# Optimization experiments

Hardware: AMD Instinct MI355X
Metric: run time of the kernel (lower is better)

The kernel has to match this reference:

```python
import jax, jax.numpy as jnp
import numpy as np

THRESHOLD = 1.0  # max tolerable Sampson error (px^2), as in the docstring example scale


def _normalize(pts, w):
    # pts: (B, M, 3) homogeneous points, w: (B, M) 0/1 weights.
    # Hartley normalization: centroid -> origin, mean distance -> sqrt(2).
    ws = w.sum(-1, keepdims=True)                                   # (B, 1)
    mean = (pts[..., :2] * w[..., None]).sum(-2) / ws               # (B, 2)
    d = jnp.linalg.norm(pts[..., :2] - mean[..., None, :], axis=-1)  # (B, M)
    md = (d * w).sum(-1) / ws[..., 0]                               # (B,)
    s = jnp.sqrt(2.0) / (md + 1e-8)
    z, o = jnp.zeros_like(s), jnp.ones_like(s)
    T = jnp.stack([
        jnp.stack([s, z, -s * mean[..., 0]], -1),
        jnp.stack([z, s, -s * mean[..., 1]], -1),
        jnp.stack([z, z, o], -1)], -2)                              # (B, 3, 3)
    return pts @ jnp.swapaxes(T, -1, -2), T


def eight_point(p1, p2, w):
    # Weighted normalized 8-point algorithm. p1, p2: (B, M, 3); w: (B, M).
    # Zero-weight rows contribute nothing to A^T A, so this equals fitting on the
    # selected subset (as the original does by fancy-indexing inlier rows).
    p1n, T1 = _normalize(p1, w)
    p2n, T2 = _normalize(p2, w)
    A = (p2n[..., :, None] * p1n[..., None, :]).reshape(p1.shape[:-2] + (-1, 9))
    A = A * w[..., None]                                            # (B, M, 9)
    AtA = jnp.einsum('...mi,...mj->...ij', A, A)                    # (B, 9, 9)
    _, V = jnp.linalg.eigh(AtA)                                     # ascending eigvals
    F = V[..., :, 0].reshape(p1.shape[:-2] + (3, 3))                # null vector
    U, S, Vt = jnp.linalg.svd(F, full_matrices=False)               # enforce rank 2
    F = (U * S.at[..., -1].set(0.0)[..., None, :]) @ Vt
    F = jnp.swapaxes(T2, -1, -2) @ F @ T1                           # denormalize
    return F / F[..., 2:3, 2:3]


def sampson_error(p1, p2, F):
    # p1, p2: (N, 3); F: (B, 3, 3) -> err: (B, N)
    Fx1 = jnp.einsum('bij,nj->bni', F, p1)
    Ftx2 = jnp.einsum('bij,ni->bnj', F, p2)
    num = jnp.einsum('ni,bni->bn', p2, Fx1) ** 2
    den = Fx1[..., 0] ** 2 + Fx1[..., 1] ** 2 + Ftx2[..., 0] ** 2 + Ftx2[..., 1] ** 2
    return num / den


def setup_inputs() -> dict:
    N, ITERS, K = 16384, 4096, 8
    rng = np.random.default_rng(0)
    X = rng.uniform(-2.0, 2.0, (N, 3)); X[:, 2] += 6.0               # 3D points, depth ~[4, 8]
    Kmat = np.array([[500.0, 0.0, 256.0], [0.0, 500.0, 256.0], [0.0, 0.0, 1.0]])
    th = 0.1
    R = np.array([[np.cos(th), 0.0, np.sin(th)], [0.0, 1.0, 0.0], [-np.sin(th), 0.0, np.cos(th)]])
    t = np.array([0.5, 0.1, 0.0])
    x1 = X @ Kmat.T; x1 /= x1[:, 2:]
    X2 = X @ R.T + t
    x2 = X2 @ Kmat.T; x2 /= x2[:, 2:]
    x1[:, :2] += rng.normal(0.0, 0.3, (N, 2))
    x2[:, :2] += rng.normal(0.0, 0.3, (N, 2))
    out = rng.random(N) < 0.3
    x2[out, :2] = rng.uniform(0.0, 512.0, (int(out.sum()), 2))
    samples = jax.random.randint(jax.random.key(0), (ITERS, K), 0, N, dtype=jnp.int32)
    return {"pts1": jnp.asarray(x1, jnp.float32), "pts2": jnp.asarray(x2, jnp.float32),
            "samples": samples, "iterations": ITERS, "num_of_select": K}


def reference(pts1, pts2, samples, iterations, num_of_select):
    samples = samples[:iterations, :num_of_select]                   # (B, 8), static slice
    # uniqueness check per hypothesis row (original drops non-unique rows; we mask them)
    srt = jnp.sort(samples, axis=-1)
    uniq = jnp.all(srt[:, 1:] != srt[:, :-1], axis=-1)               # (B,)
    p1s, p2s = pts1[samples], pts2[samples]                          # (B, 8, 3)
    w1 = jnp.ones(samples.shape, pts1.dtype)
    F = eight_point(p1s, p2s, w1)                                    # (B, 3, 3)
    err = sampson_error(pts1, pts2, F)                               # (B, N)
    inl = err <= THRESHOLD
    ml = inl.sum(-1).astype(pts1.dtype)                              # mask_lens
    ml_max = jnp.max(jnp.where(uniq, ml, 0.0))
    mask_len_ratio = ml / ml_max
    # sqrt of inlier errors; safe-guard masked entries so sqrt grad stays finite
    sqrt_sum = (jnp.sqrt(jnp.where(inl, err, 1.0)) * inl).sum(-1)
    means = (sqrt_sum + 1e-8) / (ml + 1e-8)
    means_max = jnp.max(jnp.where(uniq, means, -jnp.inf))
    score = 0.5 * mask_len_ratio + 0.5 * (1.0 - means / means_max)
    best = jnp.argmax(jnp.where(uniq, score, -jnp.inf))
    wbest = inl[best].astype(pts1.dtype)                             # (N,)
    Mbest = eight_point(pts1[None], pts2[None], wbest[None])[0]      # refit on inliers
    return Mbest, inl[best]
```

## Files before the change

### kernel.cpp

```cpp
#include <hip/hip_runtime.h>
#include <math.h>
#include <type_traits>
#include <utility>

#if defined(__has_builtin)
#if __has_builtin(__builtin_amdgcn_rcpf)
#define FAST_RCPF(x) __builtin_amdgcn_rcpf(x)
#endif
#if __has_builtin(__builtin_amdgcn_sqrtf)
#define FAST_SQRTF(x) __builtin_amdgcn_sqrtf(x)
#endif
#endif
#ifndef FAST_RCPF
#define FAST_RCPF(x) (1.0f / (x))
#endif
#ifndef FAST_SQRTF
#define FAST_SQRTF(x) sqrtf(x)
#endif

__host__ __device__ constexpr int PIX(int i, int j) { return i * (i + 1) / 2 + j; }

template <int N, int I = 0, typename F>
__device__ __forceinline__ void static_for(F&& f) {
  if constexpr (I < N) {
    f(std::integral_constant<int, I>{});
    static_for<N, I + 1>(static_cast<F&&>(f));
  }
}

template <int I, int J, int K>
__device__ __forceinline__ double csub9(const double* M, double s) {
  if constexpr (K >= J) return s;
  else return csub9<I, J, K + 1>(M, s - M[PIX(I, K)] * M[PIX(J, K)]);
}
template <int I, int J>
__device__ __forceinline__ void cholJ(double* M) {
  if constexpr (J <= I) {
    double s = csub9<I, J, 0>(M, M[PIX(I, J)]);
    if constexpr (J == I)
      M[PIX(I, I)] = sqrt(fmax(s, 1e-300));
    else
      M[PIX(I, J)] = s / M[PIX(J, J)];
    cholJ<I, J + 1>(M);
  }
}
template <int I>
__device__ __forceinline__ void cholI(double* M) {
  if constexpr (I < 9) {
    cholJ<I, 0>(M);
    cholI<I + 1>(M);
  }
}

template <int I, int K>
__device__ __forceinline__ double fsub9(const double* L, const double* x, double s) {
  if constexpr (K >= I) return s;
  else return fsub9<I, K + 1>(L, x, s - L[PIX(I, K)] * x[K]);
}
template <int I>
__device__ __forceinline__ void fwd9(const double* L, double* x) {
  if constexpr (I < 9) {
    x[I] = fsub9<I, 0>(L, x, x[I]) / L[PIX(I, I)];
    fwd9<I + 1>(L, x);
  }
}
template <int I, int K>
__device__ __forceinline__ double bsub9(const double* L, const double* x, double s) {
  if constexpr (K >= 9) return s;
  else return bsub9<I, K + 1>(L, x, s - L[PIX(K, I)] * x[K]);
}
template <int I>
__device__ __forceinline__ void bwd9(const double* L, double* x) {
  if constexpr (I >= 0) {
    x[I] = bsub9<I, I + 1>(L, x, x[I]) / L[PIX(I, I)];
    bwd9<I - 1>(L, x);
  }
}

template <int I, int J>
__device__ __forceinline__ void ataIJ(double* M, const double (&a)[9], double w) {
  if constexpr (J <= I) {
    M[PIX(I, J)] += w * a[I] * a[J];
    ataIJ<I, J + 1>(M, a, w);
  }
}
template <int I>
__device__ __forceinline__ void ataI(double* M, const double (&a)[9], double w) {
  if constexpr (I < 9) {
    ataIJ<I, 0>(M, a, w);
    ataI<I + 1>(M, a, w);
  }
}

#define JROT(P, Q)                                                              \
  {                                                                             \
    double apq = a##P##Q;                                                       \
    if (fabs(apq) >= 1e-300) {                                                  \
      double tau = (a##Q##Q - a##P##P) / (2.0 * apq);                           \
      double t = ((tau >= 0.0) ? 1.0 : -1.0) / (fabs(tau) + sqrt(1.0 + tau * tau)); \
      double c = 1.0 / sqrt(1.0 + t * t);                                       \
      double s = t * c;                                                         \
      double t0p = a0##P, t0q = a0##Q;                                          \
      a0##P = c * t0p - s * t0q; a0##Q = s * t0p + c * t0q;                     \
      double t1p = a1##P, t1q = a1##Q;                                          \
      a1##P = c * t1p - s * t1q; a1##Q = s * t1p + c * t1q;                     \
      double t2p = a2##P, t2q = a2##Q;                                          \
      a2##P = c * t2p - s * t2q; a2##Q = s * t2p + c * t2q;                     \
      double rp0 = a##P##0, rq0 = a##Q##0;                                      \
      a##P##0 = c * rp0 - s * rq0; a##Q##0 = s * rp0 + c * rq0;                 \
      double rp1 = a##P##1, rq1 = a##Q##1;                                      \
      a##P##1 = c * rp1 - s * rq1; a##Q##1 = s * rp1 + c * rq1;                 \
      double rp2 = a##P##2, rq2 = a##Q##2;                                      \
      a##P##2 = c * rp2 - s * rq2; a##Q##2 = s * rp2 + c * rq2;                 \
      double u0p = V0##P, u0q = V0##Q;                                          \
      V0##P = c * u0p - s * u0q; V0##Q = s * u0p + c * u0q;                     \
      double u1p = V1##P, u1q = V1##Q;                                          \
      V1##P = c * u1p - s * u1q; V1##Q = s * u1p + c * u1q;                     \
      double u2p = V2##P, u2q = V2##Q;                                          \
      V2##P = c * u2p - s * u2q; V2##Q = s * u2p + c * u2q;                     \
    }                                                                           \
  }

__device__ __forceinline__ void solveF(double* M, double s1, double m1x, double m1y,
                                       double s2, double m2x, double m2y,
                                       float* out) {
  double tr = M[0] + M[2] + M[5] + M[9] + M[14] + M[20] + M[27] + M[35] + M[44];
  double shift = 1e-12 * tr;
  M[0] += shift; M[2] += shift; M[5] += shift; M[9] += shift; M[14] += shift;
  M[20] += shift; M[27] += shift; M[35] += shift; M[44] += shift;
  cholI<0>(M);
  double x[9];
  static_for<9>([&](auto i) { x[i] = 1.0; });
  static_for<3>([&](auto) {
    fwd9<0>(M, x);
    bwd9<8>(M, x);
    double n = 0.0;
    static_for<9>([&](auto i) { n += x[i] * x[i]; });
    n = 1.0 / sqrt(n);
    static_for<9>([&](auto i) { x[i] *= n; });
  });
  const double g00 = x[0] * x[0] + x[3] * x[3] + x[6] * x[6];
  const double g01 = x[0] * x[1] + x[3] * x[4] + x[6] * x[7];
  const double g02 = x[0] * x[2] + x[3] * x[5] + x[6] * x[8];
  const double g11 = x[1] * x[1] + x[4] * x[4] + x[7] * x[7];
  const double g12 = x[1] * x[2] + x[4] * x[5] + x[7] * x[8];
  const double g22 = x[2] * x[2] + x[5] * x[5] + x[8] * x[8];
  double a00 = g00, a01 = g01, a02 = g02;
  double a10 = g01, a11 = g11, a12 = g12;
  double a20 = g02, a21 = g12, a22 = g22;
  double V00 = 1, V01 = 0, V02 = 0;
  double V10 = 0, V11 = 1, V12 = 0;
  double V20 = 0, V21 = 0, V22 = 1;
  for (int sweep = 0; sweep < 6; ++sweep) {
    JROT(0, 1);
    JROT(0, 2);
    JROT(1, 2);
  }
  double mv = a00, v0 = V00, v1 = V10, v2 = V20;
  if (a11 < mv) { mv = a11; v0 = V01; v1 = V11; v2 = V21; }
  if (a22 < mv) { mv = a22; v0 = V02; v1 = V12; v2 = V22; }
  const double fv0 = x[0] * v0 + x[1] * v1 + x[2] * v2;
  const double fv1 = x[3] * v0 + x[4] * v1 + x[5] * v2;
  const double fv2 = x[6] * v0 + x[7] * v1 + x[8] * v2;
  const double F200 = x[0] - fv0 * v0, F201 = x[1] - fv0 * v1, F202 = x[2] - fv0 * v2;
  const double F210 = x[3] - fv1 * v0, F211 = x[4] - fv1 * v1, F212 = x[5] - fv1 * v2;
  const double F220 = x[6] - fv2 * v0, F221 = x[7] - fv2 * v1, F222 = x[8] - fv2 * v2;
  const double R00 = s2 * F200, R01 = s2 * F201, R02 = s2 * F202;
  const double R10 = s2 * F210, R11 = s2 * F211, R12 = s2 * F212;
  const double R20 = -s2 * m2x * F200 - s2 * m2y * F210 + F220;
  const double R21 = -s2 * m2x * F201 - s2 * m2y * F211 + F221;
  const double R22 = -s2 * m2x * F202 - s2 * m2y * F212 + F222;
  const double Ff00 = s1 * R00, Ff01 = s1 * R01;
  const double Ff02 = -s1 * m1x * R00 - s1 * m1y * R01 + R02;
  const double Ff10 = s1 * R10, Ff11 = s1 * R11;
  const double Ff12 = -s1 * m1x * R10 - s1 * m1y * R11 + R12;
  const double Ff20 = s1 * R20, Ff21 = s1 * R21;
  const double Ff22 = -s1 * m1x * R20 - s1 * m1y * R21 + R22;
  const double inv = 1.0 / Ff22;
  out[0] = (float)(Ff00 * inv); out[1] = (float)(Ff01 * inv); out[2] = (float)(Ff02 * inv);
  out[3] = (float)(Ff10 * inv); out[4] = (float)(Ff11 * inv); out[5] = (float)(Ff12 * inv);
  out[6] = (float)(Ff20 * inv); out[7] = (float)(Ff21 * inv); out[8] = (float)(Ff22 * inv);
}

struct F9 {
  float f0, f1, f2, f3, f4, f5, f6, f7, f8;
};

__device__ __forceinline__ F9 loadF(const float* __restrict__ p) {
  F9 F;
  F.f0 = p[0]; F.f1 = p[1]; F.f2 = p[2];
  F.f3 = p[3]; F.f4 = p[4]; F.f5 = p[5];
  F.f6 = p[6]; F.f7 = p[7]; F.f8 = p[8];
  return F;
}

__device__ __forceinline__ void samp_numden(const F9& F, float px, float py,
                                            float qx, float qy, float& num,
                                            float& den) {
  float a0 = fmaf(F.f0, px, fmaf(F.f1, py, F.f2));
  float a1 = fmaf(F.f3, px, fmaf(F.f4, py, F.f5));
  float a2 = fmaf(F.f6, px, fmaf(F.f7, py, F.f8));
  float b0 = fmaf(F.f0, qx, fmaf(F.f3, qy, F.f6));
  float b1 = fmaf(F.f1, qx, fmaf(F.f4, qy, F.f7));
  float d = fmaf(qx, a0, fmaf(qy, a1, a2));
  num = d * d;
  den = fmaf(a0, a0, fmaf(a1, a1, fmaf(b0, b0, b1 * b1)));
}

__device__ __forceinline__ void samp_acc(const F9& F, float px, float py,
                                         float qx, float qy, float& cnt,
                                         float& ss) {
  float num, den;
  samp_numden(F, px, py, qx, qy, num, den);
  if (num <= den) {
    cnt += 1.0f;
    ss += FAST_SQRTF(num * FAST_RCPF(den));
  }
}

__global__ __launch_bounds__(256, 1) void prep_and_fit(
    const float* __restrict__ pts1, const float* __restrict__ pts2,
    const int* __restrict__ samples, float4* __restrict__ P1,
    float4* __restrict__ P2, float* __restrict__ models,
    int* __restrict__ uflag, int N, int iters, int TB) {
  if ((int)blockIdx.x < TB) {
    const int i = blockIdx.x * 256 + threadIdx.x;
    if (i < N) {
      P1[i] = make_float4(pts1[3 * i], pts1[3 * i + 1], pts1[3 * i + 2], 0.f);
      P2[i] = make_float4(pts2[3 * i], pts2[3 * i + 1], pts2[3 * i + 2], 0.f);
    }
    return;
  }
  if (threadIdx.x >= 64) return;
  const int it = (blockIdx.x - TB) * 64 + threadIdx.x;
  if (it >= iters) return;

  int idx[8];
  static_for<8>([&](auto k) { idx[k] = samples[it * 8 + k]; });
  int u = 1;
  static_for<8>([&](auto A) {
    static_for<8>([&](auto B) {
      if constexpr (decltype(B)::value > decltype(A)::value) {
        if (idx[A] == idx[B]) u = 0;
      }
    });
  });
  uflag[it] = u;

  float X1[8], Y1[8], Z1[8], X2[8], Y2[8], Z2[8];
  static_for<8>([&](auto k) {
    const int j = idx[k];
    X1[k] = pts1[3 * j]; Y1[k] = pts1[3 * j + 1]; Z1[k] = pts1[3 * j + 2];
    X2[k] = pts2[3 * j]; Y2[k] = pts2[3 * j + 1]; Z2[k] = pts2[3 * j + 2];
  });
  double sx1 = 0, sy1 = 0, sx2 = 0, sy2 = 0;
  static_for<8>([&](auto k) {
    sx1 += (double)X1[k]; sy1 += (double)Y1[k];
    sx2 += (double)X2[k]; sy2 += (double)Y2[k];
  });
  const double m1x = sx1 / 8.0, m1y = sy1 / 8.0;
  const double m2x = sx2 / 8.0, m2y = sy2 / 8.0;
  double sd1 = 0, sd2 = 0;
  static_for<8>([&](auto k) {
    double dx1 = (double)X1[k] - m1x, dy1 = (double)Y1[k] - m1y;
    double dx2 = (double)X2[k] - m2x, dy2 = (double)Y2[k] - m2y;
    sd1 += sqrt(dx1 * dx1 + dy1 * dy1);
    sd2 += sqrt(dx2 * dx2 + dy2 * dy2);
  });
  const double s1 = sqrt(2.0) / (sd1 / 8.0 + 1e-8);
  const double s2 = sqrt(2.0) / (sd2 / 8.0 + 1e-8);

  double M[45];
  static_for<45>([&](auto r) { M[r] = 0.0; });
  static_for<8>([&](auto k) {
    const double z1 = (double)Z1[k], z2 = (double)Z2[k];
    const double p1x = s1 * ((double)X1[k] - m1x * z1);
    const double p1y = s1 * ((double)Y1[k] - m1y * z1);
    const double p2x = s2 * ((double)X2[k] - m2x * z2);
    const double p2y = s2 * ((double)Y2[k] - m2y * z2);
    const double a[9] = {p2x * p1x, p2x * p1y, p2x * z1,
                         p2y * p1x, p2y * p1y, p2y * z1,
                         z2 * p1x,  z2 * p1y,  z2 * z1};
    ataI<0>(M, a, 1.0);
  });
  solveF(M, s1, m1x, m1y, s2, m2x, m2y, models + (size_t)it * 9);
}

__global__ __launch_bounds__(256, 4) void sampson_stats4(
    const float4* __restrict__ P1, const float4* __restrict__ P2,
    const float* __restrict__ models, float* __restrict__ ml,
    float* __restrict__ ssum, int N, int iters) {
  const int m0 = blockIdx.x * 4;
  const int c0 = min(m0 + 0, iters - 1), c1 = min(m0 + 1, iters - 1);
  const int c2 = min(m0 + 2, iters - 1), c3 = min(m0 + 3, iters - 1);
  const F9 Fa = loadF(models + (size_t)c0 * 9);
  const F9 Fb = loadF(models + (size_t)c1 * 9);
  const F9 Fc = loadF(models + (size_t)c2 * 9);
  const F9 Fd = loadF(models + (size_t)c3 * 9);
  float ca = 0, cb = 0, cc = 0, cd = 0;
  float sa = 0, sb = 0, sc_ = 0, sd = 0;
  const int NP = N & ~511;
  for (int i = threadIdx.x; i < NP; i += 512) {
    const float4 pA = P1[i];
    const float4 qA = P2[i];
    const float4 pB = P1[i + 256];
    const float4 qB = P2[i + 256];
    samp_acc(Fa, pA.x, pA.y, qA.x, qA.y, ca, sa);
    samp_acc(Fb, pA.x, pA.y, qA.x, qA.y, cb, sb);
    samp_acc(Fc, pA.x, pA.y, qA.x, qA.y, cc, sc_);
    samp_acc(Fd, pA.x, pA.y, qA.x, qA.y, cd, sd);
    samp_acc(Fa, pB.x, pB.y, qB.x, qB.y, ca, sa);
    samp_acc(Fb, pB.x, pB.y, qB.x, qB.y, cb, sb);
    samp_acc(Fc, pB.x, pB.y, qB.x, qB.y, cc, sc_);
    samp_acc(Fd, pB.x, pB.y, qB.x, qB.y, cd, sd);
  }
  for (int i = NP + threadIdx.x; i < N; i += 256) {
    const float4 p = P1[i];
    const float4 q = P2[i];
    samp_acc(Fa, p.x, p.y, q.x, q.y, ca, sa);
    samp_acc(Fb, p.x, p.y, q.x, q.y, cb, sb);
    samp_acc(Fc, p.x, p.y, q.x, q.y, cc, sc_);
    samp_acc(Fd, p.x, p.y, q.x, q.y, cd, sd);
  }
  __shared__ float shc[4][4], shs[4][4];
  const int lane = threadIdx.x & 63, wv = threadIdx.x >> 6;
  float c4[4] = {ca, cb, cc, cd};
  float s4[4] = {sa, sb, sc_, sd};
  static_for<4>([&](auto m) {
    float c = c4[m], s = s4[m];
#pragma unroll
    for (int o = 32; o > 0; o >>= 1) {
      c += __shfl_down(c, o);
      s += __shfl_down(s, o);
    }
    if (lane == 0) { shc[wv][m] = c; shs[wv][m] = s; }
  });
  __syncthreads();
  if (threadIdx.x < 4 && m0 + threadIdx.x < iters) {
    const int m = threadIdx.x;
    ml[m0 + m] = shc[0][m] + shc[1][m] + shc[2][m] + shc[3][m];
    ssum[m0 + m] = shs[0][m] + shs[1][m] + shs[2][m] + shs[3][m];
  }
}

__global__ __launch_bounds__(256) void select_best(
    const float* __restrict__ ml, const float* __restrict__ ssum,
    const int* __restrict__ uniq, int iters, int* __restrict__ best) {
  const int tid = threadIdx.x;
  __shared__ float ra[256], rb[256];
  __shared__ int rid[256];
  float mlmax = 0.f, mnmax = -INFINITY;
  for (int i = tid; i < iters; i += 256) {
    if (uniq[i]) {
      float m = ml[i];
      mlmax = fmaxf(mlmax, m);
      float mean = (ssum[i] + 1e-8f) / (m + 1e-8f);
      mnmax = fmaxf(mnmax, mean);
    }
  }
  ra[tid] = mlmax;
  rb[tid] = mnmax;
  __syncthreads();
  for (int s = 128; s > 0; s >>= 1) {
    if (tid < s) {
      ra[tid] = fmaxf(ra[tid], ra[tid + s]);
      rb[tid] = fmaxf(rb[tid], rb[tid + s]);
    }
    __syncthreads();
  }
  const float MLMAX = ra[0];
  const float MNMAX = rb[0];
  __syncthreads();
  float bsc = -INFINITY;
  int bid = 0x7FFFFFFF;
  for (int i = tid; i < iters; i += 256) {
    float sc = -INFINITY;
    float m = ml[i];
    float mean = (ssum[i] + 1e-8f) / (m + 1e-8f);
    if (uniq[i]) sc = 0.5f * (m / MLMAX) + 0.5f * (1.0f - mean / MNMAX);
    if (sc > bsc || (sc == bsc && i < bid)) { bsc = sc; bid = i; }
  }
  ra[tid] = bsc;
  rid[tid] = bid;
  __syncthreads();
  for (int s = 128; s > 0; s >>= 1) {
    if (tid < s) {
      if (ra[tid + s] > ra[tid] ||
          (ra[tid + s] == ra[tid] && rid[tid + s] < rid[tid])) {
        ra[tid] = ra[tid + s];
        rid[tid] = rid[tid + s];
      }
    }
    __syncthreads();
  }
  if (tid == 0) best[0] = rid[0];
}

__global__ __launch_bounds__(256) void mask_pass1(
    const float4* __restrict__ P1, const float4* __restrict__ P2,
    const float* __restrict__ models, const int* __restrict__ best,
    float* __restrict__ outmask, double* __restrict__ acc, int N) {
  const int i = blockIdx.x * 256 + threadIdx.x;
  double w = 0, a = 0, b = 0, c = 0, d = 0;
  if (i < N) {
    const F9 F = loadF(models + (size_t)best[0] * 9);
    const float4 p = P1[i];
    const float4 q = P2[i];
    float num, den;
    samp_numden(F, p.x, p.y, q.x, q.y, num, den);
    const bool in = (num <= den);
    float m = in ? 1.0f : 0.0f;
    outmask[i] = m;
    w = (double)m;
    a = w * (double)p.x;
    b = w * (double)p.y;
    c = w * (double)q.x;
    d = w * (double)q.y;
  }
#pragma unroll
  for (int o = 32; o > 0; o >>= 1) {
    w += __shfl_down(w, o); a += __shfl_down(a, o); b += __shfl_down(b, o);
    c += __shfl_down(c, o); d += __shfl_down(d, o);
  }
  if ((threadIdx.x & 63) == 0) {
    atomicAdd(&acc[0], w); atomicAdd(&acc[1], a); atomicAdd(&acc[2], b);
    atomicAdd(&acc[3], c); atomicAdd(&acc[4], d);
  }
}

__global__ __launch_bounds__(256) void ff_pass2(
    const float* __restrict__ mask, const float4* __restrict__ P1,
    const float4* __restrict__ P2, double* __restrict__ acc, int N) {
  const double WS = acc[0];
  const double M1X = acc[1] / WS, M1Y = acc[2] / WS;
  const double M2X = acc[3] / WS, M2Y = acc[4] / WS;
  const int i = blockIdx.x * 256 + threadIdx.x;
  double s1 = 0, s2 = 0;
  if (i < N) {
    double w = (double)mask[i];
    if (w != 0.0) {
      const float4 p = P1[i];
      const float4 q = P2[i];
      double dx1 = (double)p.x - M1X, dy1 = (double)p.y - M1Y;
      double dx2 = (double)q.x - M2X, dy2 = (double)q.y - M2Y;
      s1 = w * sqrt(dx1 * dx1 + dy1 * dy1);
      s2 = w * sqrt(dx2 * dx2 + dy2 * dy2);
    }
  }
#pragma unroll
  for (int o = 32; o > 0; o >>= 1) {
    s1 += __shfl_down(s1, o);
    s2 += __shfl_down(s2, o);
  }
  if ((threadIdx.x & 63) == 0) {
    atomicAdd(&acc[5], s1);
    atomicAdd(&acc[6], s2);
  }
}

__global__ __launch_bounds__(256, 1) void ff_pass3(
    const float* __restrict__ mask, const float4* __restrict__ P1,
    const float4* __restrict__ P2, double* __restrict__ acc, int N) {
  const double WS = acc[0];
  const double M1X = acc[1] / WS, M1Y = acc[2] / WS;
  const double M2X = acc[3] / WS, M2Y = acc[4] / WS;
  const double S1 = sqrt(2.0) / (acc[5] / WS + 1e-8);
  const double S2 = sqrt(2.0) / (acc[6] / WS + 1e-8);
  double A[45];
  static_for<45>([&](auto r) { A[r] = 0.0; });
#pragma unroll
  for (int k = 0; k < 4; ++k) {
    const int i = blockIdx.x * 1024 + k * 256 + threadIdx.x;
    if (i < N) {
      const double w = (double)mask[i];
      if (w != 0.0) {
        const float4 p = P1[i];
        const float4 q = P2[i];
        const double zz1 = (double)p.z, zz2 = (double)q.z;
        const double p1x = S1 * ((double)p.x - M1X * zz1);
        const double p1y = S1 * ((double)p.y - M1Y * zz1);
        const double p2x = S2 * ((double)q.x - M2X * zz2);
        const double p2y = S2 * ((double)q.y - M2Y * zz2);
        const double a[9] = {p2x * p1x, p2x * p1y, p2x * zz1,
                             p2y * p1x, p2y * p1y, p2y * zz1,
                             zz2 * p1x, zz2 * p1y, zz2 * zz1};
        const double ww = w * w;
        ataI<0>(A, a, ww);
      }
    }
  }
  const int lane = threadIdx.x & 63;
  static_for<45>([&](auto r) {
    double v = A[r];
#pragma unroll
    for (int o = 32; o > 0; o >>= 1) v += __shfl_down(v, o);
    if (lane == 0) atomicAdd(&acc[7 + r], v);
  });
}

__global__ __launch_bounds__(64, 1) void ff_solve(const double* __restrict__ acc,
                                                  float* __restrict__ outF) {
  if (threadIdx.x != 0 || blockIdx.x != 0) return;
  const double WS = acc[0];
  const double M1X = acc[1] / WS, M1Y = acc[2] / WS;
  const double M2X = acc[3] / WS, M2Y = acc[4] / WS;
  const double S1 = sqrt(2.0) / (acc[5] / WS + 1e-8);
  const double S2 = sqrt(2.0) / (acc[6] / WS + 1e-8);
  double M[45];
  static_for<45>([&](auto r) { M[r] = acc[7 + r]; });
  solveF(M, S1, M1X, M1Y, S2, M2X, M2Y, outF);
}

extern "C" void kernel_launch(void* const* d_in, const int* in_sizes, int n_in,
                              void* d_out, int out_size, void* d_ws, size_t ws_size,
                              hipStream_t stream) {
  const float* pts1 = (const float*)d_in[0];
  const float* pts2 = (const float*)d_in[1];
  const int* samples = (const int*)d_in[2];
  const int N = in_sizes[0] / 3;
  const int iters = in_sizes[2] / 8;

  float4* P1 = (float4*)d_ws;
  float4* P2 = P1 + N;
  double* acc = (double*)(P2 + N);
  float* models = (float*)(acc + 52);
  float* ml = models + (size_t)iters * 9;
  float* ssum = ml + iters;
  int* uniq = (int*)(ssum + iters);
  int* best = uniq + iters;

  float* outF = (float*)d_out;
  float* outmask = outF + 9;

  const int TB = (N + 255) / 256;
  const int FB = (iters + 63) / 64;
  hipMemsetAsync(acc, 0, 52 * sizeof(double), stream);
  prep_and_fit<<<TB + FB, 256, 0, stream>>>(pts1, pts2, samples, P1, P2,
                                            models, uniq, N, iters, TB);
  sampson_stats4<<<(iters + 3) / 4, 256, 0, stream>>>(P1, P2, models, ml, ssum,
                                                      N, iters);
  select_best<<<1, 256, 0, stream>>>(ml, ssum, uniq, iters, best);
  mask_pass1<<<(N + 255) / 256, 256, 0, stream>>>(P1, P2, models, best, outmask,
                                                  acc, N);
  ff_pass2<<<(N + 255) / 256, 256, 0, stream>>>(outmask, P1, P2, acc, N);
  ff_pass3<<<(N + 1023) / 1024, 256, 0, stream>>>(outmask, P1, P2, acc, N);
  ff_solve<<<1, 64, 0, stream>>>(acc, outF);
}
```

Measured before the change: 198.7 us.

## Fuse selection into mask pass and merge refit passes with last-block solve

Replaces the separate best-model selection kernel with a per-block redundant reduction inside the mask kernel. The centroid-distance pass and the A^T A accumulation are merged into one pass by accumulating on centered coordinates and rescaling afterwards, and the final solve runs in the last block via an atomic ticket. The accumulator memset is folded into the first kernel, and the Sampson sqrt(num/den) is replaced by |d|*rsqrt(den) without branching. Together these cut launch count and serial latency, at the cost of every mask block redoing the 4096-entry selection reduction and slightly different floating-point rounding.

```diff
diff --git a/kernel.cpp b/kernel.cpp
--- a/kernel.cpp
+++ b/kernel.cpp
@@ -7,15 +7,15 @@
 #if __has_builtin(__builtin_amdgcn_rcpf)
 #define FAST_RCPF(x) __builtin_amdgcn_rcpf(x)
 #endif
-#if __has_builtin(__builtin_amdgcn_sqrtf)
-#define FAST_SQRTF(x) __builtin_amdgcn_sqrtf(x)
+#if __has_builtin(__builtin_amdgcn_rsqf)
+#define FAST_RSQF(x) __builtin_amdgcn_rsqf(x)
 #endif
 #endif
 #ifndef FAST_RCPF
 #define FAST_RCPF(x) (1.0f / (x))
 #endif
-#ifndef FAST_SQRTF
-#define FAST_SQRTF(x) sqrtf(x)
+#ifndef FAST_RSQF
+#define FAST_RSQF(x) (1.0f / sqrtf(x))
 #endif
 
 __host__ __device__ constexpr int PIX(int i, int j) { return i * (i + 1) / 2 + j; }
@@ -196,7 +196,7 @@
 
 __device__ __forceinline__ void samp_numden(const F9& F, float px, float py,
                                             float qx, float qy, float& num,
-                                            float& den) {
+                                            float& den, float& dout) {
   float a0 = fmaf(F.f0, px, fmaf(F.f1, py, F.f2));
   float a1 = fmaf(F.f3, px, fmaf(F.f4, py, F.f5));
   float a2 = fmaf(F.f6, px, fmaf(F.f7, py, F.f8));
@@ -205,25 +205,31 @@
   float d = fmaf(qx, a0, fmaf(qy, a1, a2));
   num = d * d;
   den = fmaf(a0, a0, fmaf(a1, a1, fmaf(b0, b0, b1 * b1)));
+  dout = d;
 }
 
 __device__ __forceinline__ void samp_acc(const F9& F, float px, float py,
                                          float qx, float qy, float& cnt,
                                          float& ss) {
-  float num, den;
-  samp_numden(F, px, py, qx, qy, num, den);
-  if (num <= den) {
-    cnt += 1.0f;
-    ss += FAST_SQRTF(num * FAST_RCPF(den));
-  }
+  float num, den, d;
+  samp_numden(F, px, py, qx, qy, num, den, d);
+  const bool in = (num <= den);
+  const float val = fabsf(d) * FAST_RSQF(den);
+  cnt += in ? 1.0f : 0.0f;
+  ss += in ? val : 0.0f;
 }
 
 __global__ __launch_bounds__(256, 1) void prep_and_fit(
     const float* __restrict__ pts1, const float* __restrict__ pts2,
     const int* __restrict__ samples, float4* __restrict__ P1,
     float4* __restrict__ P2, float* __restrict__ models,
-    int* __restrict__ uflag, int N, int iters, int TB) {
+    int* __restrict__ uflag, double* __restrict__ acc,
+    unsigned int* __restrict__ ticket, int N, int iters, int TB) {
   if ((int)blockIdx.x < TB) {
+    if (blockIdx.x == 0) {
+      if (threadIdx.x < 52) acc[threadIdx.x] = 0.0;
+      if (threadIdx.x == 52) *ticket = 0u;
+    }
     const int i = blockIdx.x * 256 + threadIdx.x;
     if (i < N) {
       P1[i] = make_float4(pts1[3 * i], pts1[3 * i + 1], pts1[3 * i + 2], 0.f);
@@ -343,9 +349,11 @@
   }
 }
 
-__global__ __launch_bounds__(256) void select_best(
-    const float* __restrict__ ml, const float* __restrict__ ssum,
-    const int* __restrict__ uniq, int iters, int* __restrict__ best) {
+__global__ __launch_bounds__(256) void selmask_p1(
+    const float4* __restrict__ P1, const float4* __restrict__ P2,
+    const float* __restrict__ models, const float* __restrict__ ml,
+    const float* __restrict__ ssum, const int* __restrict__ uniq,
+    float* __restrict__ outmask, double* __restrict__ acc, int N, int iters) {
   const int tid = threadIdx.x;
   __shared__ float ra[256], rb[256];
   __shared__ int rid[256];
@@ -393,21 +401,16 @@
     }
     __syncthreads();
   }
-  if (tid == 0) best[0] = rid[0];
-}
-
-__global__ __launch_bounds__(256) void mask_pass1(
-    const float4* __restrict__ P1, const float4* __restrict__ P2,
-    const float* __restrict__ models, const int* __restrict__ best,
-    float* __restrict__ outmask, double* __restrict__ acc, int N) {
-  const int i = blockIdx.x * 256 + threadIdx.x;
+  const int best = rid[0];
+
+  const int i = blockIdx.x * 256 + tid;
   double w = 0, a = 0, b = 0, c = 0, d = 0;
   if (i < N) {
-    const F9 F = loadF(models + (size_t)best[0] * 9);
+    const F9 F = loadF(models + (size_t)best * 9);
     const float4 p = P1[i];
     const float4 q = P2[i];
-    float num, den;
-    samp_numden(F, p.x, p.y, q.x, q.y, num, den);
+    float num, den, dd;
+    samp_numden(F, p.x, p.y, q.x, q.y, num, den, dd);
     const bool in = (num <= den);
     float m = in ? 1.0f : 0.0f;
     outmask[i] = m;
@@ -422,50 +425,21 @@
     w += __shfl_down(w, o); a += __shfl_down(a, o); b += __shfl_down(b, o);
     c += __shfl_down(c, o); d += __shfl_down(d, o);
   }
-  if ((threadIdx.x & 63) == 0) {
+  if ((tid & 63) == 0) {
     atomicAdd(&acc[0], w); atomicAdd(&acc[1], a); atomicAdd(&acc[2], b);
     atomicAdd(&acc[3], c); atomicAdd(&acc[4], d);
   }
 }
 
-__global__ __launch_bounds__(256) void ff_pass2(
+__global__ __launch_bounds__(256, 1) void ff_p23_solve(
     const float* __restrict__ mask, const float4* __restrict__ P1,
-    const float4* __restrict__ P2, double* __restrict__ acc, int N) {
+    const float4* __restrict__ P2, double* __restrict__ acc,
+    unsigned int* __restrict__ ticket, float* __restrict__ outF, int N,
+    int NB) {
   const double WS = acc[0];
   const double M1X = acc[1] / WS, M1Y = acc[2] / WS;
   const double M2X = acc[3] / WS, M2Y = acc[4] / WS;
-  const int i = blockIdx.x * 256 + threadIdx.x;
-  double s1 = 0, s2 = 0;
-  if (i < N) {
-    double w = (double)mask[i];
-    if (w != 0.0) {
-      const float4 p = P1[i];
-      const float4 q = P2[i];
-      double dx1 = (double)p.x - M1X, dy1 = (double)p.y - M1Y;
-      double dx2 = (double)q.x - M2X, dy2 = (double)q.y - M2Y;
-      s1 = w * sqrt(dx1 * dx1 + dy1 * dy1);
-      s2 = w * sqrt(dx2 * dx2 + dy2 * dy2);
-    }
-  }
-#pragma unroll
-  for (int o = 32; o > 0; o >>= 1) {
-    s1 += __shfl_down(s1, o);
-    s2 += __shfl_down(s2, o);
-  }
-  if ((threadIdx.x & 63) == 0) {
-    atomicAdd(&acc[5], s1);
-    atomicAdd(&acc[6], s2);
-  }
-}
-
-__global__ __launch_bounds__(256, 1) void ff_pass3(
-    const float* __restrict__ mask, const float4* __restrict__ P1,
-    const float4* __restrict__ P2, double* __restrict__ acc, int N) {
-  const double WS = acc[0];
-  const double M1X = acc[1] / WS, M1Y = acc[2] / WS;
-  const double M2X = acc[3] / WS, M2Y = acc[4] / WS;
-  const double S1 = sqrt(2.0) / (acc[5] / WS + 1e-8);
-  const double S2 = sqrt(2.0) / (acc[6] / WS + 1e-8);
+  double sd1 = 0, sd2 = 0;
   double A[45];
   static_for<45>([&](auto r) { A[r] = 0.0; });
 #pragma unroll
@@ -476,39 +450,61 @@
       if (w != 0.0) {
         const float4 p = P1[i];
         const float4 q = P2[i];
-        const double zz1 = (double)p.z, zz2 = (double)q.z;
-        const double p1x = S1 * ((double)p.x - M1X * zz1);
-        const double p1y = S1 * ((double)p.y - M1Y * zz1);
-        const double p2x = S2 * ((double)q.x - M2X * zz2);
-        const double p2y = S2 * ((double)q.y - M2Y * zz2);
-        const double a[9] = {p2x * p1x, p2x * p1y, p2x * zz1,
-                             p2y * p1x, p2y * p1y, p2y * zz1,
-                             zz2 * p1x, zz2 * p1y, zz2 * zz1};
-        const double ww = w * w;
-        ataI<0>(A, a, ww);
+        const double v0 = (double)p.x - M1X, v1 = (double)p.y - M1Y;
+        const double u0 = (double)q.x - M2X, u1 = (double)q.y - M2Y;
+        sd1 += sqrt(v0 * v0 + v1 * v1);
+        sd2 += sqrt(u0 * u0 + u1 * u1);
+        const double a[9] = {u0 * v0, u0 * v1, u0,
+                             u1 * v0, u1 * v1, u1,
+                             v0,      v1,      1.0};
+        ataI<0>(A, a, 1.0);
       }
     }
   }
   const int lane = threadIdx.x & 63;
+  {
+    double t1 = sd1, t2 = sd2;
+#pragma unroll
+    for (int o = 32; o > 0; o >>= 1) {
+      t1 += __shfl_down(t1, o);
+      t2 += __shfl_down(t2, o);
+    }
+    if (lane == 0) {
+      atomicAdd(&acc[5], t1);
+      atomicAdd(&acc[6], t2);
+    }
+  }
   static_for<45>([&](auto r) {
     double v = A[r];
 #pragma unroll
     for (int o = 32; o > 0; o >>= 1) v += __shfl_down(v, o);
     if (lane == 0) atomicAdd(&acc[7 + r], v);
   });
-}
-
-__global__ __launch_bounds__(64, 1) void ff_solve(const double* __restrict__ acc,
-                                                  float* __restrict__ outF) {
-  if (threadIdx.x != 0 || blockIdx.x != 0) return;
-  const double WS = acc[0];
-  const double M1X = acc[1] / WS, M1Y = acc[2] / WS;
-  const double M2X = acc[3] / WS, M2Y = acc[4] / WS;
-  const double S1 = sqrt(2.0) / (acc[5] / WS + 1e-8);
-  const double S2 = sqrt(2.0) / (acc[6] / WS + 1e-8);
-  double M[45];
-  static_for<45>([&](auto r) { M[r] = acc[7 + r]; });
-  solveF(M, S1, M1X, M1Y, S2, M2X, M2Y, outF);
+  __syncthreads();
+  __threadfence();
+  if (threadIdx.x == 0) {
+    const unsigned int t = atomicAdd(ticket, 1u);
+    if (t == (unsigned int)(NB - 1)) {
+      const double SD1 = atomicAdd(&acc[5], 0.0);
+      const double SD2 = atomicAdd(&acc[6], 0.0);
+      const double S1 = sqrt(2.0) / (SD1 / WS + 1e-8);
+      const double S2 = sqrt(2.0) / (SD2 / WS + 1e-8);
+      double M[45];
+      static_for<45>([&](auto r) { M[r] = atomicAdd(&acc[7 + r], 0.0); });
+      static_for<9>([&](auto R) {
+        static_for<9>([&](auto C) {
+          constexpr int r = decltype(R)::value;
+          constexpr int c = decltype(C)::value;
+          if constexpr (c <= r) {
+            const double sr = ((r / 3) < 2 ? S2 : 1.0) * ((r % 3) < 2 ? S1 : 1.0);
+            const double sc = ((c / 3) < 2 ? S2 : 1.0) * ((c % 3) < 2 ? S1 : 1.0);
+            M[PIX(r, c)] *= sr * sc;
+          }
+        });
+      });
+      solveF(M, S1, M1X, M1Y, S2, M2X, M2Y, outF);
+    }
+  }
 }
 
 extern "C" void kernel_launch(void* const* d_in, const int* in_sizes, int n_in,
@@ -523,26 +519,25 @@
   float4* P1 = (float4*)d_ws;
   float4* P2 = P1 + N;
   double* acc = (double*)(P2 + N);
-  float* models = (float*)(acc + 52);
+  unsigned int* ticket = (unsigned int*)(acc + 52);
+  float* models = (float*)(ticket + 4);
   float* ml = models + (size_t)iters * 9;
   float* ssum = ml + iters;
   int* uniq = (int*)(ssum + iters);
-  int* best = uniq + iters;
 
   float* outF = (float*)d_out;
   float* outmask = outF + 9;
 
   const int TB = (N + 255) / 256;
   const int FB = (iters + 63) / 64;
-  hipMemsetAsync(acc, 0, 52 * sizeof(double), stream);
+  const int NB = (N + 1023) / 1024;
   prep_and_fit<<<TB + FB, 256, 0, stream>>>(pts1, pts2, samples, P1, P2,
-                                            models, uniq, N, iters, TB);
+                                            models, uniq, acc, ticket, N,
+                                            iters, TB);
   sampson_stats4<<<(iters + 3) / 4, 256, 0, stream>>>(P1, P2, models, ml, ssum,
                                                       N, iters);
-  select_best<<<1, 256, 0, stream>>>(ml, ssum, uniq, iters, best);
-  mask_pass1<<<(N + 255) / 256, 256, 0, stream>>>(P1, P2, models, best, outmask,
-                                                  acc, N);
-  ff_pass2<<<(N + 255) / 256, 256, 0, stream>>>(outmask, P1, P2, acc, N);
-  ff_pass3<<<(N + 1023) / 1024, 256, 0, stream>>>(outmask, P1, P2, acc, N);
-  ff_solve<<<1, 64, 0, stream>>>(acc, outF);
-}
+  selmask_p1<<<(N + 255) / 256, 256, 0, stream>>>(P1, P2, models, ml, ssum,
+                                                  uniq, outmask, acc, N, iters);
+  ff_p23_solve<<<NB, 256, 0, stream>>>(outmask, P1, P2, acc, ticket, outF, N,
+                                       NB);
+}
```

Result: no change. 196.4 us (-1.2%).
